# Performance work log

Measured on AMD Instinct MI355X. Metric: run time of the kernel, lower is better.

The kernel has to match this reference:

```python
import jax, jax.numpy as jnp
import numpy as np
import math

HASHMAP_SIZE = 1 << 17
N_LEVELS = 16
N_FEATURES = 2
BASE_RES = 16.0
GROWTH = 1.5  # per-level resolution growth factor
PRIME_Y = np.uint32(2654435761)  # Instant-NGP spatial hash prime


def hash_encode(x, encoding):
    """Multiresolution 2D hash-grid encoding with bilinear interpolation.
    x: [N, 2] in [0,1); encoding: [T, L, F]. Returns [N, L*F]."""
    N = x.shape[0]
    scales = jnp.asarray(BASE_RES * GROWTH ** np.arange(N_LEVELS),
                         dtype=x.dtype)  # [L]
    pos = x[:, None, :] * scales[None, :, None]        # [N, L, 2]
    pf = jnp.floor(pos)
    frac = pos - pf                                    # [N, L, 2]
    pi = pf.astype(jnp.uint32)                         # integer corner base
    lvl = jnp.arange(N_LEVELS)[None, :]                # [1, L]

    feat = jnp.zeros((N, N_LEVELS, N_FEATURES), dtype=x.dtype)
    for cx in (0, 1):
        for cy in (0, 1):
            ix = pi[..., 0] + jnp.uint32(cx)
            iy = pi[..., 1] + jnp.uint32(cy)
            h = ix ^ (iy * PRIME_Y)                    # spatial hash (wraps mod 2^32)
            idx = (h & jnp.uint32(HASHMAP_SIZE - 1)).astype(jnp.int32)  # [N, L]
            wx = frac[..., 0] if cx else 1.0 - frac[..., 0]
            wy = frac[..., 1] if cy else 1.0 - frac[..., 1]
            feat = feat + (wx * wy)[..., None] * encoding[idx, lvl]  # gather [N,L,F]
    return feat.reshape(N, N_LEVELS * N_FEATURES)


def setup_inputs() -> dict:
    key = jax.random.key(0)
    ks = jax.random.split(key, 8)
    N = 1 << 20
    n_neurons = [32, 64, 64, 3]
    x = jax.random.uniform(ks[0], (N, 2), dtype=jnp.float32)
    # encoding init: rand * 2e-4 - 1e-4
    encoding = jax.random.uniform(ks[1], (HASHMAP_SIZE, N_LEVELS, N_FEATURES),
                                  dtype=jnp.float32) * 2e-4 - 1e-4
    inp = {"x": x, "encoding": encoding}
    for i in range(3):
        s = 1.0 / math.sqrt(n_neurons[i])
        w = jax.random.uniform(ks[2 + i], (n_neurons[i], n_neurons[i + 1]),
                               dtype=jnp.float32) * 2 * s - s
        b = jax.random.uniform(ks[5 + i], (n_neurons[i + 1],),
                               dtype=jnp.float32) * 2 * s - s
        inp[f"w{i}"] = w
        inp[f"b{i}"] = b
    return inp


def reference(x, encoding, w0, b0, w1, b1, w2, b2):
    feat = hash_encode(x, encoding)                 # [N, 32]
    h = jax.nn.relu(feat @ w0 + b0)                 # [N, 64]
    h = jax.nn.relu(h @ w1 + b1)                    # [N, 64]
    return h @ w2 + b2                              # [N, 3]
```

## Files before the change

### kernel.cpp

```cpp
#include <hip/hip_runtime.h>
#include <stdint.h>

typedef __bf16 bf16_t;
typedef bf16_t bf16x8 __attribute__((ext_vector_type(8)));
typedef float  f32x4  __attribute__((ext_vector_type(4)));
typedef float  f32x2v __attribute__((ext_vector_type(2)));

static constexpr uint32_t PRIME = 2654435761u;
static constexpr uint32_t HMASK = (1u << 17) - 1u;
static constexpr uint32_t TSIZE = 1u << 17;

static constexpr int NLDS   = 5308;
static constexpr int NDALL  = 136642;

static constexpr float FSCALE = 8192.0f;
static constexpr float WSCALE = 1.0f / 8192.0f;

__device__ __forceinline__ uint32_t fbits(float f) {
    union { float f; uint32_t u; } v; v.f = f; return v.u;
}
__device__ __forceinline__ float asfloat(uint32_t u) {
    union { uint32_t u; float f; } v; v.u = u; return v.f;
}

__device__ __forceinline__ uint32_t enc8(float v) {
    const uint32_t s = (fbits(v) >> 24) & 0x80u;
    float m = fabsf(v) * 0x1p-120f;
    uint32_t u = fbits(m);
    u += 0x7FFFFu + ((u >> 20) & 1u);
    return s | ((u >> 20) & 0x7fu);
}
__device__ __forceinline__ uint32_t pack8(float a, float b) {
#if __has_builtin(__builtin_amdgcn_cvt_pk_fp8_f32)
    return (uint32_t)__builtin_amdgcn_cvt_pk_fp8_f32(a, b, 0, false) & 0xffffu;
#else
    return enc8(a) | (enc8(b) << 8);
#endif
}
__device__ __forceinline__ float2 unpack8(uint32_t u) {
#if __has_builtin(__builtin_amdgcn_cvt_pk_f32_fp8)
    f32x2v r = __builtin_amdgcn_cvt_pk_f32_fp8((int)u, false);
    return make_float2(r.x, r.y);
#else
    const float f0 = asfloat(((u & 0x80u) << 24) | ((u & 0x7fu) << 20)) * 0x1p120f;
    const float f1 = asfloat(((u & 0x8000u) << 16) | ((u & 0x7f00u) << 12)) * 0x1p120f;
    return make_float2(f0, f1);
#endif
}

__global__ __launch_bounds__(256)
void repack_enc8(const float2* __restrict__ src, uint16_t* __restrict__ dst) {
    __shared__ uint16_t ldsT[8 * 257];
    const int tid = threadIdx.x;
    const int t0  = blockIdx.x * 256;
#pragma unroll
    for (int k = 0; k < 8; ++k) {
        const int j = k * 256 + tid;
        const int tl = j >> 3, l8 = j & 7;
        const float2 f = src[((size_t)(t0 + tl) << 4) + 8 + l8];
        ldsT[l8 * 257 + tl] = (uint16_t)pack8(f.x * FSCALE, f.y * FSCALE);
    }
    __syncthreads();
#pragma unroll
    for (int k = 0; k < 8; ++k)
        dst[((uint32_t)k << 17) + t0 + tid] = ldsT[k * 257 + tid];
}

__global__ __launch_bounds__(256)
void densify_enc(const float2* __restrict__ src, uint16_t* __restrict__ dst) {
    const int i = blockIdx.x * 256 + threadIdx.x;
    if (i >= NDALL) return;
    int lvl, W, off;
    if      (i <   289) { lvl = 0; W =  17; off = 0;     }
    else if (i <   914) { lvl = 1; W =  25; off = 289;   }
    else if (i <  2283) { lvl = 2; W =  37; off = 914;   }
    else if (i <  5308) { lvl = 3; W =  55; off = 2283;  }
    else if (i < 12032) { lvl = 4; W =  82; off = 5308;  }
    else if (i < 27161) { lvl = 5; W = 123; off = 12032; }
    else if (i < 61017) { lvl = 6; W = 184; off = 27161; }
    else                { lvl = 7; W = 275; off = 61017; }
    const int li = i - off;
    const uint32_t iy = (uint32_t)(li / W), ix = (uint32_t)(li % W);
    const uint32_t h = (ix ^ (iy * PRIME)) & HMASK;
    const float2 f = src[h * 16 + lvl];
    dst[i] = (uint16_t)pack8(f.x * FSCALE, f.y * FSCALE);
}

__global__ __launch_bounds__(256, 2)
void fused_hash_mlp(const float* __restrict__ xin,
                    const uint16_t* __restrict__ tab8,
                    const uint16_t* __restrict__ dense,
                    const float* __restrict__ w0, const float* __restrict__ b0,
                    const float* __restrict__ w1, const float* __restrict__ b1,
                    const float* __restrict__ w2, const float* __restrict__ b2,
                    float* __restrict__ out,
                    int nGroups)
{
    __shared__ uint16_t ldsTab[NLDS];
    __shared__ __align__(16) bf16_t lds[4 * 16 * 80];

    const int tid  = threadIdx.x;
    const int wib  = tid >> 6;
    const int lane = tid & 63;
    const int q    = lane >> 4;
    const int n16  = lane & 15;

    bf16_t* myLds = &lds[wib * (16 * 80)];

    for (int i = tid; i < NLDS; i += 256) ldsTab[i] = dense[i];

    bf16x8 Bw0[4], Bw1[2][4], Bw2[2];
#pragma unroll
    for (int t = 0; t < 4; ++t)
#pragma unroll
        for (int j = 0; j < 8; ++j)
            Bw0[t][j] = (bf16_t)(w0[(q * 8 + j) * 64 + t * 16 + n16] * WSCALE);
#pragma unroll
    for (int c = 0; c < 2; ++c)
#pragma unroll
        for (int t = 0; t < 4; ++t)
#pragma unroll
            for (int j = 0; j < 8; ++j)
                Bw1[c][t][j] = (bf16_t)w1[(c * 32 + q * 8 + j) * 64 + t * 16 + n16];
#pragma unroll
    for (int c = 0; c < 2; ++c)
#pragma unroll
        for (int j = 0; j < 8; ++j)
            Bw2[c][j] = (n16 < 3) ? (bf16_t)w2[(c * 32 + q * 8 + j) * 3 + n16]
                                  : (bf16_t)0.0f;

    float bv0[4], bv1[4];
#pragma unroll
    for (int t = 0; t < 4; ++t) {
        bv0[t] = b0[t * 16 + n16];
        bv1[t] = b1[t * 16 + n16];
    }
    const float bv2 = (n16 < 3) ? b2[n16] : 0.0f;

    const float sb = 16.0f * ((q == 0) ? 1.0f :
                              (q == 1) ? 5.0625f :
                              (q == 2) ? 25.62890625f :
                                         129.746337890625f);
    const float sc[4] = { sb, sb * 1.5f, sb * 2.25f, sb * 3.375f };

    const uint32_t l8base = ((uint32_t)((q >= 2 ? q - 2 : 0) * 4)) << 17;

    __syncthreads();

    for (int g = blockIdx.x; g < nGroups; g += gridDim.x) {
        const int tile = g * 4 + wib;
        const int p = tile * 16 + n16;
        const float2 xy = ((const float2*)xin)[p];
        const float px = xy.x, py = xy.y;

        bf16x8 af;
#pragma unroll
        for (int lv = 0; lv < 4; ++lv) {
            const float posx = px * sc[lv], posy = py * sc[lv];
            const float fx = floorf(posx), fy = floorf(posy);
            const float frx = posx - fx,  fry = posy - fy;
            const uint32_t ix = (uint32_t)fx, iy = (uint32_t)fy;

            const uint32_t Wl = (lv == 0) ? 17u  : (lv == 1) ? 25u
                              : (lv == 2) ? 37u  : 55u;
            const uint32_t Ol = (lv == 0) ? 0u   : (lv == 1) ? 289u
                              : (lv == 2) ? 914u : 2283u;
            const uint32_t Wg = (lv == 0) ? 82u    : (lv == 1) ? 123u
                              : (lv == 2) ? 184u   : 275u;
            const uint32_t Og = (lv == 0) ? 5308u  : (lv == 1) ? 12032u
                              : (lv == 2) ? 27161u : 61017u;

            uint32_t u00, u10, u01, u11;
            if (q == 0) {
                const uint32_t a = Ol + iy * Wl + ix;
                u00 = ldsTab[a];
                u10 = ldsTab[a + 1];
                u01 = ldsTab[a + Wl];
                u11 = ldsTab[a + Wl + 1];
            } else if (q == 1) {
                const uint32_t a = Og + iy * Wg + ix;
                u00 = dense[a];
                u10 = dense[a + 1];
                u01 = dense[a + Wg];
                u11 = dense[a + Wg + 1];
            } else {
                const uint32_t hy0 = iy * PRIME, hy1 = hy0 + PRIME;
                const uint32_t i00 = ( ix       ^ hy0) & HMASK;
                const uint32_t i10 = ((ix + 1u) ^ hy0) & HMASK;
                const uint32_t i01 = ( ix       ^ hy1) & HMASK;
                const uint32_t i11 = ((ix + 1u) ^ hy1) & HMASK;
                const uint32_t base = l8base + ((uint32_t)lv << 17);
                u00 = tab8[base + i00];
                u10 = tab8[base + i10];
                u01 = tab8[base + i01];
                u11 = tab8[base + i11];
            }

            const float2 e00 = unpack8(u00);
            const float2 e10 = unpack8(u10);
            const float2 e01 = unpack8(u01);
            const float2 e11 = unpack8(u11);
            const float wx1 = frx, wx0 = 1.0f - frx, wy1 = fry, wy0 = 1.0f - fry;
            const float w00 = wx0 * wy0, w10 = wx1 * wy0, w01 = wx0 * wy1, w11 = wx1 * wy1;
            const float f0 = w00 * e00.x + w10 * e10.x + w01 * e01.x + w11 * e11.x;
            const float f1 = w00 * e00.y + w10 * e10.y + w01 * e01.y + w11 * e11.y;
            af[2 * lv]     = (bf16_t)f0;
            af[2 * lv + 1] = (bf16_t)f1;
        }

        f32x4 c0[4];
#pragma unroll
        for (int t = 0; t < 4; ++t) {
            f32x4 cc = { bv0[t], bv0[t], bv0[t], bv0[t] };
            c0[t] = __builtin_amdgcn_mfma_f32_16x16x32_bf16(af, Bw0[t], cc, 0, 0, 0);
        }

#pragma unroll
        for (int t = 0; t < 4; ++t)
#pragma unroll
            for (int r = 0; r < 4; ++r)
                myLds[(q * 4 + r) * 80 + t * 16 + n16] = (bf16_t)fmaxf(c0[t][r], 0.0f);

        bf16x8 A1[2];
#pragma unroll
        for (int c = 0; c < 2; ++c)
            A1[c] = *(const bf16x8*)&myLds[n16 * 80 + c * 32 + q * 8];

        f32x4 c1[4];
#pragma unroll
        for (int t = 0; t < 4; ++t) {
            f32x4 cc = { bv1[t], bv1[t], bv1[t], bv1[t] };
            cc    = __builtin_amdgcn_mfma_f32_16x16x32_bf16(A1[0], Bw1[0][t], cc, 0, 0, 0);
            c1[t] = __builtin_amdgcn_mfma_f32_16x16x32_bf16(A1[1], Bw1[1][t], cc, 0, 0, 0);
        }

#pragma unroll
        for (int t = 0; t < 4; ++t)
#pragma unroll
            for (int r = 0; r < 4; ++r)
                myLds[(q * 4 + r) * 80 + t * 16 + n16] = (bf16_t)fmaxf(c1[t][r], 0.0f);

        bf16x8 A2[2];
#pragma unroll
        for (int c = 0; c < 2; ++c)
            A2[c] = *(const bf16x8*)&myLds[n16 * 80 + c * 32 + q * 8];

        f32x4 co = { bv2, bv2, bv2, bv2 };
        co = __builtin_amdgcn_mfma_f32_16x16x32_bf16(A2[0], Bw2[0], co, 0, 0, 0);
        co = __builtin_amdgcn_mfma_f32_16x16x32_bf16(A2[1], Bw2[1], co, 0, 0, 0);

        if (n16 < 3) {
#pragma unroll
            for (int r = 0; r < 4; ++r)
                out[(size_t)(tile * 16 + q * 4 + r) * 3 + n16] = co[r];
        }
    }
}

__global__ __launch_bounds__(256)
void fused_hash_mlp_fp32(const float* __restrict__ xin,
                         const float* __restrict__ enc,
                         const float* __restrict__ w0, const float* __restrict__ b0,
                         const float* __restrict__ w1, const float* __restrict__ b1,
                         const float* __restrict__ w2, const float* __restrict__ b2,
                         float* __restrict__ out,
                         int nGroups)
{
    __shared__ __align__(16) bf16_t lds[4 * 16 * 80];
    const int tid  = threadIdx.x;
    const int wib  = tid >> 6;
    const int lane = tid & 63;
    const int q    = lane >> 4;
    const int n16  = lane & 15;
    bf16_t* myLds = &lds[wib * (16 * 80)];

    bf16x8 Bw0[4], Bw1[2][4], Bw2[2];
#pragma unroll
    for (int t = 0; t < 4; ++t)
#pragma unroll
        for (int j = 0; j < 8; ++j)
            Bw0[t][j] = (bf16_t)w0[(q * 8 + j) * 64 + t * 16 + n16];
#pragma unroll
    for (int c = 0; c < 2; ++c)
#pragma unroll
        for (int t = 0; t < 4; ++t)
#pragma unroll
            for (int j = 0; j < 8; ++j)
                Bw1[c][t][j] = (bf16_t)w1[(c * 32 + q * 8 + j) * 64 + t * 16 + n16];
#pragma unroll
    for (int c = 0; c < 2; ++c)
#pragma unroll
        for (int j = 0; j < 8; ++j)
            Bw2[c][j] = (n16 < 3) ? (bf16_t)w2[(c * 32 + q * 8 + j) * 3 + n16]
                                  : (bf16_t)0.0f;

    float bv0[4], bv1[4];
#pragma unroll
    for (int t = 0; t < 4; ++t) { bv0[t] = b0[t * 16 + n16]; bv1[t] = b1[t * 16 + n16]; }
    const float bv2 = (n16 < 3) ? b2[n16] : 0.0f;

    const float sb = 16.0f * ((q == 0) ? 1.0f : (q == 1) ? 5.0625f :
                              (q == 2) ? 25.62890625f : 129.746337890625f);
    const float sc[4] = { sb, sb * 1.5f, sb * 2.25f, sb * 3.375f };
    const char* encB = (const char*)enc;
    const uint32_t lvBase = (uint32_t)q * 32u;

    for (int g = blockIdx.x; g < nGroups; g += gridDim.x) {
        const int tile = g * 4 + wib;
        const int p = tile * 16 + n16;
        const float2 xy = ((const float2*)xin)[p];
        const float px = xy.x, py = xy.y;

        bf16x8 af;
#pragma unroll
        for (int lv = 0; lv < 4; ++lv) {
            const float posx = px * sc[lv], posy = py * sc[lv];
            const float fx = floorf(posx), fy = floorf(posy);
            const float frx = posx - fx,  fry = posy - fy;
            const uint32_t ix = (uint32_t)fx, iy = (uint32_t)fy;
            const uint32_t hy0 = iy * PRIME, hy1 = hy0 + PRIME;
            const uint32_t i00 = ( ix       ^ hy0) & HMASK;
            const uint32_t i10 = ((ix + 1u) ^ hy0) & HMASK;
            const uint32_t i01 = ( ix       ^ hy1) & HMASK;
            const uint32_t i11 = ((ix + 1u) ^ hy1) & HMASK;
            const uint32_t off = lvBase + (uint32_t)lv * 8u;
            const float2 e00 = *(const float2*)(encB + (i00 * 128u + off));
            const float2 e10 = *(const float2*)(encB + (i10 * 128u + off));
            const float2 e01 = *(const float2*)(encB + (i01 * 128u + off));
            const float2 e11 = *(const float2*)(encB + (i11 * 128u + off));
            const float wx1 = frx, wx0 = 1.0f - frx, wy1 = fry, wy0 = 1.0f - fry;
            const float w00 = wx0 * wy0, w10 = wx1 * wy0, w01 = wx0 * wy1, w11 = wx1 * wy1;
            af[2 * lv]     = (bf16_t)(w00 * e00.x + w10 * e10.x + w01 * e01.x + w11 * e11.x);
            af[2 * lv + 1] = (bf16_t)(w00 * e00.y + w10 * e10.y + w01 * e01.y + w11 * e11.y);
        }

        f32x4 c0[4];
#pragma unroll
        for (int t = 0; t < 4; ++t) {
            f32x4 cc = { bv0[t], bv0[t], bv0[t], bv0[t] };
            c0[t] = __builtin_amdgcn_mfma_f32_16x16x32_bf16(af, Bw0[t], cc, 0, 0, 0);
        }
        __syncthreads();
#pragma unroll
        for (int t = 0; t < 4; ++t)
#pragma unroll
            for (int r = 0; r < 4; ++r)
                myLds[(q * 4 + r) * 80 + t * 16 + n16] = (bf16_t)fmaxf(c0[t][r], 0.0f);
        __syncthreads();
        bf16x8 A1[2];
#pragma unroll
        for (int c = 0; c < 2; ++c)
            A1[c] = *(const bf16x8*)&myLds[n16 * 80 + c * 32 + q * 8];

        f32x4 c1[4];
#pragma unroll
        for (int t = 0; t < 4; ++t) {
            f32x4 cc = { bv1[t], bv1[t], bv1[t], bv1[t] };
            cc    = __builtin_amdgcn_mfma_f32_16x16x32_bf16(A1[0], Bw1[0][t], cc, 0, 0, 0);
            c1[t] = __builtin_amdgcn_mfma_f32_16x16x32_bf16(A1[1], Bw1[1][t], cc, 0, 0, 0);
        }
        __syncthreads();
#pragma unroll
        for (int t = 0; t < 4; ++t)
#pragma unroll
            for (int r = 0; r < 4; ++r)
                myLds[(q * 4 + r) * 80 + t * 16 + n16] = (bf16_t)fmaxf(c1[t][r], 0.0f);
        __syncthreads();
        bf16x8 A2[2];
#pragma unroll
        for (int c = 0; c < 2; ++c)
            A2[c] = *(const bf16x8*)&myLds[n16 * 80 + c * 32 + q * 8];

        f32x4 co = { bv2, bv2, bv2, bv2 };
        co = __builtin_amdgcn_mfma_f32_16x16x32_bf16(A2[0], Bw2[0], co, 0, 0, 0);
        co = __builtin_amdgcn_mfma_f32_16x16x32_bf16(A2[1], Bw2[1], co, 0, 0, 0);
        if (n16 < 3) {
#pragma unroll
            for (int r = 0; r < 4; ++r)
                out[(size_t)(tile * 16 + q * 4 + r) * 3 + n16] = co[r];
        }
    }
}

extern "C" void kernel_launch(void* const* d_in, const int* in_sizes, int n_in,
                              void* d_out, int out_size, void* d_ws, size_t ws_size,
                              hipStream_t stream) {
    const float* x  = (const float*)d_in[0];
    const float* en = (const float*)d_in[1];
    const float* w0 = (const float*)d_in[2];
    const float* b0 = (const float*)d_in[3];
    const float* w1 = (const float*)d_in[4];
    const float* b1 = (const float*)d_in[5];
    const float* w2 = (const float*)d_in[6];
    const float* b2 = (const float*)d_in[7];
    float* out = (float*)d_out;

    const int N = in_sizes[0] / 2;
    const int nTiles = N / 16;
    const int nGroups = nTiles / 4;

    const size_t wsNeeded = ((size_t)TSIZE * 8 + NDALL) * 2;
    if (ws_size >= wsNeeded) {
        uint16_t* tab8  = (uint16_t*)d_ws;
        uint16_t* dense = tab8 + ((size_t)TSIZE * 8);
        repack_enc8<<<TSIZE / 256, 256, 0, stream>>>((const float2*)en, tab8);
        densify_enc<<<(NDALL + 255) / 256, 256, 0, stream>>>((const float2*)en, dense);
        int blocks = 2048;
        if (blocks > nGroups) blocks = nGroups;
        fused_hash_mlp<<<blocks, 256, 0, stream>>>(x, tab8, dense,
                                                   w0, b0, w1, b1, w2, b2, out, nGroups);
    } else {
        int blocks = 2048;
        if (blocks > nGroups) blocks = nGroups;
        fused_hash_mlp_fp32<<<blocks, 256, 0, stream>>>(x, en, w0, b0, w1, b1, w2, b2, out, nGroups);
    }
}
```

Baseline: 201.8 us.

## Merge prepass kernels and swizzle per-wave LDS activation staging layout

Merges the two table-preparation kernels into one launch that branches on block index, which removes one kernel launch and its gap. The per-wave LDS staging buffer for MLP activations moves from a padded 80-element row stride to a 64-element stride with an XOR swizzle on both the scalar writes and the 16-byte reads. The swizzle is meant to avoid bank conflicts while using less LDS. It also templates the fp8 unpack for a future high-half variant that is not yet used.

```diff
diff --git a/kernel.cpp b/kernel.cpp
--- a/kernel.cpp
+++ b/kernel.cpp
@@ -37,53 +37,55 @@
     return enc8(a) | (enc8(b) << 8);
 #endif
 }
-__device__ __forceinline__ float2 unpack8(uint32_t u) {
+template <bool HI>
+__device__ __forceinline__ float2 unpack8w(uint32_t u) {
 #if __has_builtin(__builtin_amdgcn_cvt_pk_f32_fp8)
-    f32x2v r = __builtin_amdgcn_cvt_pk_f32_fp8((int)u, false);
+    f32x2v r = __builtin_amdgcn_cvt_pk_f32_fp8((int)u, HI);
     return make_float2(r.x, r.y);
 #else
-    const float f0 = asfloat(((u & 0x80u) << 24) | ((u & 0x7fu) << 20)) * 0x1p120f;
-    const float f1 = asfloat(((u & 0x8000u) << 16) | ((u & 0x7f00u) << 12)) * 0x1p120f;
+    const uint32_t w = HI ? (u >> 16) : (u & 0xffffu);
+    const float f0 = asfloat(((w & 0x80u) << 24) | ((w & 0x7fu) << 20)) * 0x1p120f;
+    const float f1 = asfloat(((w & 0x8000u) << 16) | ((w & 0x7f00u) << 12)) * 0x1p120f;
     return make_float2(f0, f1);
 #endif
 }
 
 __global__ __launch_bounds__(256)
-void repack_enc8(const float2* __restrict__ src, uint16_t* __restrict__ dst) {
+void prepass_all(const float2* __restrict__ src, uint16_t* __restrict__ tab8,
+                 uint16_t* __restrict__ dense) {
     __shared__ uint16_t ldsT[8 * 257];
     const int tid = threadIdx.x;
-    const int t0  = blockIdx.x * 256;
-#pragma unroll
-    for (int k = 0; k < 8; ++k) {
-        const int j = k * 256 + tid;
-        const int tl = j >> 3, l8 = j & 7;
-        const float2 f = src[((size_t)(t0 + tl) << 4) + 8 + l8];
-        ldsT[l8 * 257 + tl] = (uint16_t)pack8(f.x * FSCALE, f.y * FSCALE);
+    if (blockIdx.x < 512) {
+        const int t0 = blockIdx.x * 256;
+#pragma unroll
+        for (int k = 0; k < 8; ++k) {
+            const int j = k * 256 + tid;
+            const int tl = j >> 3, l8 = j & 7;
+            const float2 f = src[((size_t)(t0 + tl) << 4) + 8 + l8];
+            ldsT[l8 * 257 + tl] = (uint16_t)pack8(f.x * FSCALE, f.y * FSCALE);
+        }
+        __syncthreads();
+#pragma unroll
+        for (int k = 0; k < 8; ++k)
+            tab8[((uint32_t)k << 17) + t0 + tid] = ldsT[k * 257 + tid];
+    } else {
+        const int i = (blockIdx.x - 512) * 256 + tid;
+        if (i >= NDALL) return;
+        int lvl, W, off;
+        if      (i <   289) { lvl = 0; W =  17; off = 0;     }
+        else if (i <   914) { lvl = 1; W =  25; off = 289;   }
+        else if (i <  2283) { lvl = 2; W =  37; off = 914;   }
+        else if (i <  5308) { lvl = 3; W =  55; off = 2283;  }
+        else if (i < 12032) { lvl = 4; W =  82; off = 5308;  }
+        else if (i < 27161) { lvl = 5; W = 123; off = 12032; }
+        else if (i < 61017) { lvl = 6; W = 184; off = 27161; }
+        else                { lvl = 7; W = 275; off = 61017; }
+        const int li = i - off;
+        const uint32_t iy = (uint32_t)(li / W), ix = (uint32_t)(li % W);
+        const uint32_t h = (ix ^ (iy * PRIME)) & HMASK;
+        const float2 f = src[h * 16 + lvl];
+        dense[i] = (uint16_t)pack8(f.x * FSCALE, f.y * FSCALE);
     }
-    __syncthreads();
-#pragma unroll
-    for (int k = 0; k < 8; ++k)
-        dst[((uint32_t)k << 17) + t0 + tid] = ldsT[k * 257 + tid];
-}
-
-__global__ __launch_bounds__(256)
-void densify_enc(const float2* __restrict__ src, uint16_t* __restrict__ dst) {
-    const int i = blockIdx.x * 256 + threadIdx.x;
-    if (i >= NDALL) return;
-    int lvl, W, off;
-    if      (i <   289) { lvl = 0; W =  17; off = 0;     }
-    else if (i <   914) { lvl = 1; W =  25; off = 289;   }
-    else if (i <  2283) { lvl = 2; W =  37; off = 914;   }
-    else if (i <  5308) { lvl = 3; W =  55; off = 2283;  }
-    else if (i < 12032) { lvl = 4; W =  82; off = 5308;  }
-    else if (i < 27161) { lvl = 5; W = 123; off = 12032; }
-    else if (i < 61017) { lvl = 6; W = 184; off = 27161; }
-    else                { lvl = 7; W = 275; off = 61017; }
-    const int li = i - off;
-    const uint32_t iy = (uint32_t)(li / W), ix = (uint32_t)(li % W);
-    const uint32_t h = (ix ^ (iy * PRIME)) & HMASK;
-    const float2 f = src[h * 16 + lvl];
-    dst[i] = (uint16_t)pack8(f.x * FSCALE, f.y * FSCALE);
 }
 
 __global__ __launch_bounds__(256, 2)
@@ -97,15 +99,17 @@
                     int nGroups)
 {
     __shared__ uint16_t ldsTab[NLDS];
-    __shared__ __align__(16) bf16_t lds[4 * 16 * 80];
+    __shared__ __align__(16) bf16_t lds[4 * 16 * 64];
 
     const int tid  = threadIdx.x;
     const int wib  = tid >> 6;
     const int lane = tid & 63;
     const int q    = lane >> 4;
     const int n16  = lane & 15;
-
-    bf16_t* myLds = &lds[wib * (16 * 80)];
+    const int m7   = n16 & 7;
+    const int mb   = n16 >> 3;
+
+    bf16_t* myLds = &lds[wib * (16 * 64)];
 
     for (int i = tid; i < NLDS; i += 256) ldsTab[i] = dense[i];
 
@@ -144,6 +148,13 @@
     const float sc[4] = { sb, sb * 1.5f, sb * 2.25f, sb * 3.375f };
 
     const uint32_t l8base = ((uint32_t)((q >= 2 ? q - 2 : 0) * 4)) << 17;
+
+    int wbase[4];
+#pragma unroll
+    for (int r = 0; r < 4; ++r)
+        wbase[r] = (q * 4 + r) * 64 + m7 + ((mb ^ (r & 1)) << 3) + ((q & 1) << 5);
+    const int rIdx0 = n16 * 64 + (( q      ^ m7) << 3);
+    const int rIdx1 = n16 * 64 + (((4 + q) ^ m7) << 3);
 
     __syncthreads();
 
@@ -196,10 +207,10 @@
                 u11 = tab8[base + i11];
             }
 
-            const float2 e00 = unpack8(u00);
-            const float2 e10 = unpack8(u10);
-            const float2 e01 = unpack8(u01);
-            const float2 e11 = unpack8(u11);
+            const float2 e00 = unpack8w<false>(u00);
+            const float2 e10 = unpack8w<false>(u10);
+            const float2 e01 = unpack8w<false>(u01);
+            const float2 e11 = unpack8w<false>(u11);
             const float wx1 = frx, wx0 = 1.0f - frx, wy1 = fry, wy0 = 1.0f - fry;
             const float w00 = wx0 * wy0, w10 = wx1 * wy0, w01 = wx0 * wy1, w11 = wx1 * wy1;
             const float f0 = w00 * e00.x + w10 * e10.x + w01 * e01.x + w11 * e11.x;
@@ -218,13 +229,14 @@
 #pragma unroll
         for (int t = 0; t < 4; ++t)
 #pragma unroll
-            for (int r = 0; r < 4; ++r)
-                myLds[(q * 4 + r) * 80 + t * 16 + n16] = (bf16_t)fmaxf(c0[t][r], 0.0f);
-
+            for (int r = 0; r < 4; ++r) {
+                const int idx = ((t < 2) ? wbase[r] : (wbase[r] ^ 32))
+                              + ((((t & 1) ^ ((r >> 1) & 1))) << 4);
+                myLds[idx] = (bf16_t)fmaxf(c0[t][r], 0.0f);
+            }
         bf16x8 A1[2];
-#pragma unroll
-        for (int c = 0; c < 2; ++c)
-            A1[c] = *(const bf16x8*)&myLds[n16 * 80 + c * 32 + q * 8];
+        A1[0] = *(const bf16x8*)&myLds[rIdx0];
+        A1[1] = *(const bf16x8*)&myLds[rIdx1];
 
         f32x4 c1[4];
 #pragma unroll
@@ -237,13 +249,14 @@
 #pragma unroll
         for (int t = 0; t < 4; ++t)
 #pragma unroll
-            for (int r = 0; r < 4; ++r)
-                myLds[(q * 4 + r) * 80 + t * 16 + n16] = (bf16_t)fmaxf(c1[t][r], 0.0f);
-
+            for (int r = 0; r < 4; ++r) {
+                const int idx = ((t < 2) ? wbase[r] : (wbase[r] ^ 32))
+                              + ((((t & 1) ^ ((r >> 1) & 1))) << 4);
+                myLds[idx] = (bf16_t)fmaxf(c1[t][r], 0.0f);
+            }
         bf16x8 A2[2];
-#pragma unroll
-        for (int c = 0; c < 2; ++c)
-            A2[c] = *(const bf16x8*)&myLds[n16 * 80 + c * 32 + q * 8];
+        A2[0] = *(const bf16x8*)&myLds[rIdx0];
+        A2[1] = *(const bf16x8*)&myLds[rIdx1];
 
         f32x4 co = { bv2, bv2, bv2, bv2 };
         co = __builtin_amdgcn_mfma_f32_16x16x32_bf16(A2[0], Bw2[0], co, 0, 0, 0);
@@ -403,8 +416,8 @@
     if (ws_size >= wsNeeded) {
         uint16_t* tab8  = (uint16_t*)d_ws;
         uint16_t* dense = tab8 + ((size_t)TSIZE * 8);
-        repack_enc8<<<TSIZE / 256, 256, 0, stream>>>((const float2*)en, tab8);
-        densify_enc<<<(NDALL + 255) / 256, 256, 0, stream>>>((const float2*)en, dense);
+        const int preBlocks = 512 + (NDALL + 255) / 256;
+        prepass_all<<<preBlocks, 256, 0, stream>>>((const float2*)en, tab8, dense);
         int blocks = 2048;
         if (blocks > nGroups) blocks = nGroups;
         fused_hash_mlp<<<blocks, 256, 0, stream>>>(x, tab8, dense,
```

New measurement: 198.9 us. Within noise of the previous version (-1.4%).
